# Optimization experiments

Hardware: AMD Instinct MI355X
Metric: run time of the kernel (lower is better)

The kernel has to match this reference:

```python
import jax, jax.numpy as jnp
import numpy as np
import itertools

D_FEAT = 8      # feature dim per point
N_NBR = 16     # kNN neighbors (self.N)
ORDERS = (2, 3)
BIG = 99999999.0


def _to_select(N, order):
    # rows: [0] + each (order-1)-combination of {1..N-1}, first N-1 rows
    rows = [[0] + list(c) for c in itertools.combinations(range(1, N), order - 1)][:N - 1]
    return np.asarray(rows, dtype=np.int32)  # (N-1, order)


def setup_inputs() -> dict:
    key = jax.random.key(0)
    ks = jax.random.split(key, 18)
    B, NP, DM, DO, NM, PNM = 4, 4096, 16, 8, 64, 64
    r = lambda k, s: jax.random.normal(k, s, dtype=jnp.float32)
    return {
        "x": r(ks[0], (B, NP * D_FEAT)),
        "z": r(ks[1], (B, PNM)),
        "Wm2": r(ks[2], (2, DM)) * 0.5, "bm2": r(ks[3], (DM,)) * 0.1,
        "Wm3": r(ks[4], (3, DM)) * 0.5, "bm3": r(ks[5], (DM,)) * 0.1,
        "Wv2": r(ks[6], (2, DM)) * 0.5, "bv2": r(ks[7], (DM,)) * 0.1,
        "Wv3": r(ks[8], (3, DM)) * 0.5, "bv3": r(ks[9], (DM,)) * 0.1,
        "Wmx": r(ks[10], (2 * DM, DO)) * 0.1, "bmx": r(ks[11], (DO,)) * 0.1,
        "Wvx": r(ks[12], (2 * DM, NM)) * 0.1, "bvx": r(ks[13], (NM,)) * 0.1,
        "Wmz": r(ks[14], (PNM, DO)) * 0.1, "bmz": r(ks[15], (DO,)) * 0.1,
        "Wvz": r(ks[16], (PNM, NM)) * 0.1, "bvz": r(ks[17], (NM,)) * 0.1,
    }


def _forward(x, z, Wm2, bm2, Wm3, bm3, Wv2, bv2, Wv3, bv3,
             Wmx, bmx, Wvx, bvx, Wmz, bmz, Wvz, bvz):
    B = x.shape[0]
    NP = x.shape[1] // D_FEAT
    N = N_NBR
    x3 = x.reshape(B, NP, D_FEAT)

    # pairwise euclidean distances via gram trick (avoids B*NP*NP*D intermediate)
    n2 = jnp.sum(x3 * x3, axis=-1)                                   # (B, NP)
    d2 = n2[:, :, None] + n2[:, None, :] - 2.0 * jnp.einsum('bid,bjd->bij', x3, x3)
    dist = jnp.sqrt(jnp.maximum(d2, 0.0))                            # (B, NP, NP)
    dist = jnp.where(dist == 0.0, BIG, dist)                         # mask exact-zero distances
    diag = jnp.arange(NP)
    dist = dist.at[:, diag, diag].set(BIG)                           # self-distance (exactly 0 in torch)

    # N smallest, sorted ascending
    _, idx = jax.lax.top_k(-dist, N)                                 # idx: (B, NP, N)

    def order_feats(Wf, bf, order):
        ts = jnp.asarray(_to_select(N, order))                       # (N-1, order)
        sel = idx[:, :, ts]                                          # (B, NP, N-1, o)
        g = jax.vmap(lambda xb, sb: xb[sb])(x3, sel)                 # (B, NP, N-1, o, D)
        # Linear(order -> d_Mfeat) applied per feature-dim o-tuple, relu, mean over feature dims
        y = jax.nn.relu(jnp.einsum('bnrod,ok->bnrdk', g, Wf) + bf)   # (B, NP, N-1, D, K)
        return y.mean(axis=3).reshape(B, NP * (N - 1), -1)           # (B, NP*(N-1), K)

    moments = jnp.concatenate([order_feats(Wm2, bm2, 2), order_feats(Wm3, bm3, 3)], axis=-1)
    v_moments = jnp.concatenate([order_feats(Wv2, bv2, 2), order_feats(Wv3, bv3, 3)], axis=-1)

    d_out = Wmx.shape[1]
    x_new = jax.nn.relu(moments @ Wmx + bmx + (z @ Wmz + bmz)[:, None, :])
    x_new = x_new.reshape(B, NP, N - 1, d_out).mean(axis=2).reshape(B, NP * d_out)

    z_new = jax.nn.relu(v_moments @ Wvx + bvx + (z @ Wvz + bvz)[:, None, :]).mean(axis=1)
    return x_new, z_new


def reference(x, z, Wm2, bm2, Wm3, bm3, Wv2, bv2, Wv3, bv3,
              Wmx, bmx, Wvx, bvx, Wmz, bmz, Wvz, bvz):
    return _forward(x, z, Wm2, bm2, Wm3, bm3, Wv2, bv2, Wv3, bv3,
                    Wmx, bmx, Wvx, bvx, Wmz, bmz, Wvz, bvz)
```

## Files before the change

### kernel.cpp

```cpp
#include <hip/hip_runtime.h>
#include <hip/hip_bf16.h>

#define NPP 4096
#define BB 4
#define NQ 4
#define CAP 128

typedef float f32x2 __attribute__((ext_vector_type(2)));
typedef unsigned long long u64;

__device__ __forceinline__ f32x2 pk_fma(f32x2 a, f32x2 b, f32x2 c) {
    f32x2 d;
    asm("v_pk_fma_f32 %0, %1, %2, %3" : "=v"(d) : "v"(a), "v"(b), "v"(c));
    return d;
}

template <typename T>
__device__ __forceinline__ T bitonic_sort64(T v, int lane) {
    #pragma unroll
    for (int k = 2; k <= 64; k <<= 1) {
        #pragma unroll
        for (int j = k >> 1; j > 0; j >>= 1) {
            T p = __shfl_xor(v, j);
            bool up  = ((lane & k) == 0);
            bool low = ((lane & j) == 0);
            T mn = (v < p) ? v : p;
            T mx = (v < p) ? p : v;
            v = (up == low) ? mn : mx;
        }
    }
    return v;
}

__device__ __forceinline__ float dot8_pk(const f32x2* qp, f32x2 p0, f32x2 p1,
                                         f32x2 p2, f32x2 p3) {
    f32x2 acc = {0.f, 0.f};
    acc = pk_fma(qp[0], p0, acc);
    acc = pk_fma(qp[1], p1, acc);
    acc = pk_fma(qp[2], p2, acc);
    acc = pk_fma(qp[3], p3, acc);
    return acc.x + acc.y;
}


__global__ __launch_bounds__(256) void n2_kernel(
    const float* __restrict__ x, const float* __restrict__ z,
    const float* __restrict__ Wmz, const float* __restrict__ bmz,
    const float* __restrict__ Wvz, const float* __restrict__ bvz,
    float* __restrict__ n2tab, float* __restrict__ zzm, float* __restrict__ zzv,
    float* __restrict__ zout)
{
    int i = blockIdx.x * 256 + threadIdx.x;
    const float4* p = (const float4*)(x + (long)i * 8);
    float4 a = p[0], c = p[1];
    float s = 0.f;
    s = fmaf(a.x, a.x, s); s = fmaf(a.y, a.y, s);
    s = fmaf(a.z, a.z, s); s = fmaf(a.w, a.w, s);
    s = fmaf(c.x, c.x, s); s = fmaf(c.y, c.y, s);
    s = fmaf(c.z, c.z, s); s = fmaf(c.w, c.w, s);
    n2tab[i] = s;

    if (blockIdx.x == 0) {
        zout[threadIdx.x] = 0.f;
        int b = threadIdx.x >> 6, l = threadIdx.x & 63;
        float sv = 0.f;
        for (int q = 0; q < 64; ++q) sv = fmaf(z[b * 64 + q], Wvz[q * 64 + l], sv);
        zzv[b * 64 + l] = sv + bvz[l];
        if (threadIdx.x < 32) {
            int bm = threadIdx.x >> 3, lm = threadIdx.x & 7;
            float sm = 0.f;
            for (int q = 0; q < 64; ++q) sm = fmaf(z[bm * 64 + q], Wmz[q * 8 + lm], sm);
            zzm[bm * 8 + lm] = sm + bmz[lm];
        }
    }
}


__global__ __launch_bounds__(256) void fused_kernel(
    const float* __restrict__ x, const float* __restrict__ n2tab,
    const float* __restrict__ Wm2, const float* __restrict__ bm2,
    const float* __restrict__ Wm3, const float* __restrict__ bm3,
    const float* __restrict__ Wv2, const float* __restrict__ bv2,
    const float* __restrict__ Wv3, const float* __restrict__ bv3,
    const float* __restrict__ Wmx, const float* __restrict__ bmx,
    const float* __restrict__ Wvx, const float* __restrict__ bvx,
    const float* __restrict__ zzm, const float* __restrict__ zzv,
    float* __restrict__ xout, float* __restrict__ zout)
{
    __shared__ __align__(16) char ubuf[4][4352];
    __shared__ float xg_s[4][NQ][16][8];
    __shared__ int   idx_s[4][NQ][16];
    __shared__ float wmxT_s[8][40];
    __shared__ float bzm_s[8];
    __shared__ float zpart[4][64];
    __shared__ unsigned cnt_s[4][NQ];

    int lane = threadIdx.x & 63;
    int wid  = threadIdx.x >> 6;
    int gw   = blockIdx.x * 4 + wid;
    int q0   = gw * NQ;
    int b    = q0 >> 12;
    int qloc = q0 & 4095;
    const float* xb = x + (long)b * NPP * 8;
    const float* nb = n2tab + b * NPP;

    if (threadIdx.x < 256) wmxT_s[threadIdx.x & 7][threadIdx.x >> 3] = Wmx[threadIdx.x];
    if (threadIdx.x < 8)   bzm_s[threadIdx.x] = bmx[threadIdx.x] + zzm[b * 8 + threadIdx.x];
    if (lane < NQ) cnt_s[wid][lane] = 0;
    __syncthreads();

    f32x2 qp[NQ][4];
    float n2i[NQ];
    int selfT[NQ], selfL[NQ];
    #pragma unroll
    for (int q = 0; q < NQ; ++q) {
        const f32x2* qsrc = (const f32x2*)(xb + (long)(qloc + q) * 8);
        #pragma unroll
        for (int e = 0; e < 4; ++e) qp[q][e] = qsrc[e];
        n2i[q]   = nb[qloc + q];
        selfT[q] = (qloc + q) >> 6;
        selfL[q] = (qloc + q) & 63;
    }

    unsigned minb[NQ];
    #pragma unroll
    for (int q = 0; q < NQ; ++q) minb[q] = 0xFFFFFFFFu;

    #pragma unroll 4
    for (int tt = 0; tt < 32; ++tt) {
        int t = tt * 2;
        int j = t * 64 + lane;
        const f32x2* pj = (const f32x2*)(xb + (long)j * 8);
        f32x2 p0 = pj[0], p1 = pj[1], p2 = pj[2], p3 = pj[3];
        float n2j = nb[j];
        #pragma unroll
        for (int q = 0; q < NQ; ++q) {
            float dot = dot8_pk(qp[q], p0, p1, p2, p3);
            float d2  = fmaf(-2.0f, dot, n2i[q] + n2j);
            unsigned kb = __float_as_uint(d2);
            if (t == selfT[q]) kb = (lane == selfL[q]) ? 0xFFFFFFFFu : kb;
            minb[q] = (kb < minb[q]) ? kb : minb[q];
        }
    }

    unsigned T[NQ];
    #pragma unroll
    for (int q = 0; q < NQ; ++q) {
        unsigned s = bitonic_sort64(minb[q], lane);
        T[q] = (unsigned)__shfl((int)s, 15);
    }

    u64* cand = (u64*)ubuf[wid];
    #pragma unroll 2
    for (int t = 0; t < 64; ++t) {
        int j = t * 64 + lane;
        const f32x2* pj = (const f32x2*)(xb + (long)j * 8);
        f32x2 p0 = pj[0], p1 = pj[1], p2 = pj[2], p3 = pj[3];
        float n2j = nb[j];
        #pragma unroll
        for (int q = 0; q < NQ; ++q) {
            float dot = dot8_pk(qp[q], p0, p1, p2, p3);
            float d2  = fmaf(-2.0f, dot, n2i[q] + n2j);
            unsigned kb = __float_as_uint(d2);
            if (t == selfT[q]) kb = (lane == selfL[q]) ? 0xFFFFFFFFu : kb;
            if (kb <= T[q]) {
                unsigned old = atomicAdd(&cnt_s[wid][q], 1u);
                if (old < CAP) cand[q * CAP + old] = ((u64)kb << 32) | (unsigned)j;
            }
        }
    }

    #pragma unroll 1
    for (int q = 0; q < NQ; ++q) {
        unsigned nc = cnt_s[wid][q];
        int n = nc > CAP ? CAP : (int)nc;
        u64 v = (lane < n) ? cand[q * CAP + lane] : ~0ull;
        u64 R = bitonic_sort64(v, lane);
        if (n > 64) {
            u64 w2 = (64 + lane < n) ? cand[q * CAP + 64 + lane] : ~0ull;
            w2 = bitonic_sort64(w2, lane);
            u64 vt = __shfl(w2, lane - 16);
            u64 comb = (lane < 16) ? R : ((lane < 32) ? vt : ~0ull);
            R = bitonic_sort64(comb, lane);
        }
        if (lane < 16) idx_s[wid][q][lane] = (int)(R & 0xFFFFFFFFull);
    }

    #pragma unroll
    for (int p = 0; p < NQ; ++p) {
        if (lane < 16) {
            int id = idx_s[wid][p][lane];
            const float4* ps = (const float4*)(xb + (long)id * 8);
            float4 A = ps[0], C = ps[1];
            *((float4*)&xg_s[wid][p][lane][0]) = A;
            *((float4*)&xg_s[wid][p][lane][4]) = C;
        }
    }

    int k = lane & 15;
    float w20 = Wm2[k], w21 = Wm2[16 + k], bb2 = bm2[k];
    float w30 = Wm3[k], w31 = Wm3[16 + k], w32 = Wm3[32 + k], bb3 = bm3[k];
    float u20 = Wv2[k], u21 = Wv2[16 + k], cc2 = bv2[k];
    float u30 = Wv3[k], u31 = Wv3[16 + k], u32 = Wv3[32 + k], cc3 = bv3[k];

    int g  = lane >> 5;
    int nm = lane & 31;
    f32x2 wa2[16], wb2[16];
    #pragma unroll
    for (int cc = 0; cc < 16; ++cc) {
        wa2[cc].x = Wvx[(2 * cc) * 64 + nm];
        wa2[cc].y = Wvx[(2 * cc + 1) * 64 + nm];
        wb2[cc].x = Wvx[(2 * cc) * 64 + nm + 32];
        wb2[cc].y = Wvx[(2 * cc + 1) * 64 + nm + 32];
    }
    float bz3a = bvx[nm]      + zzv[b * 64 + nm];
    float bz3b = bvx[nm + 32] + zzv[b * 64 + nm + 32];

    float* mo = (float*)ubuf[wid];
    float Aacc = 0.f, Bacc = 0.f;

    #pragma unroll 1
    for (int p = 0; p < NQ; ++p) {
        float4 g0l = *(const float4*)&xg_s[wid][p][0][0];
        float4 g0h = *(const float4*)&xg_s[wid][p][0][4];
        float g0[8] = {g0l.x, g0l.y, g0l.z, g0l.w, g0h.x, g0h.y, g0h.z, g0h.w};

        #pragma unroll
        for (int pp = 0; pp < 4; ++pp) {
            int rg = lane >> 4;
            int r  = pp * 4 + rg;
            int rc = (r < 14) ? r : 14;
            int i2  = rc + 1;
            int i3a = (rc < 14) ? 1 : 2;
            int i3b = (rc < 14) ? rc + 2 : 3;
            float4 a1 = *(const float4*)&xg_s[wid][p][i2][0];
            float4 b1 = *(const float4*)&xg_s[wid][p][i2][4];
            float4 aa = *(const float4*)&xg_s[wid][p][i3a][0];
            float4 ba = *(const float4*)&xg_s[wid][p][i3a][4];
            float4 ab = *(const float4*)&xg_s[wid][p][i3b][0];
            float4 bb = *(const float4*)&xg_s[wid][p][i3b][4];
            float G1[8]  = {a1.x, a1.y, a1.z, a1.w, b1.x, b1.y, b1.z, b1.w};
            float G3a[8] = {aa.x, aa.y, aa.z, aa.w, ba.x, ba.y, ba.z, ba.w};
            float G3b[8] = {ab.x, ab.y, ab.z, ab.w, bb.x, bb.y, bb.z, bb.w};
            float s2 = 0.f, s3 = 0.f, t2 = 0.f, t3 = 0.f;
            #pragma unroll
            for (int d = 0; d < 8; ++d) {
                float gz = g0[d], g1 = G1[d], ga = G3a[d], gb = G3b[d];
                float y2 = fmaf(gz, w20, fmaf(g1, w21, bb2));
                s2 += fmaxf(y2, 0.f);
                float y3 = fmaf(gz, w30, fmaf(ga, w31, fmaf(gb, w32, bb3)));
                s3 += fmaxf(y3, 0.f);
                float z2 = fmaf(gz, u20, fmaf(g1, u21, cc2));
                t2 += fmaxf(z2, 0.f);
                float z3 = fmaf(gz, u30, fmaf(ga, u31, fmaf(gb, u32, cc3)));
                t3 += fmaxf(z3, 0.f);
            }
            if (r < 15) {
                mo[r * 72 + k]      = s2 * 0.125f;
                mo[r * 72 + 16 + k] = s3 * 0.125f;
                mo[r * 72 + 32 + k] = t2 * 0.125f;
                mo[r * 72 + 48 + k] = t3 * 0.125f;
            }
        }

        float xa = 0.f;
        #pragma unroll
        for (int half = 0; half < 2; ++half) {
            int r   = (lane >> 3) + half * 8;
            int doo = lane & 7;
            if (r < 15) {
                const f32x2* vp = (const f32x2*)&mo[r * 72];
                const f32x2* wp = (const f32x2*)&wmxT_s[doo][0];
                f32x2 acc = {0.f, 0.f};
                #pragma unroll
                for (int cc = 0; cc < 16; ++cc) acc = pk_fma(vp[cc], wp[cc], acc);
                float s = bzm_s[doo] + acc.x + acc.y;
                xa += fmaxf(s, 0.f);
            }
        }
        xa += __shfl_xor(xa, 8);
        xa += __shfl_xor(xa, 16);
        xa += __shfl_xor(xa, 32);
        if (lane < 8) xout[(long)(q0 + p) * 8 + lane] = xa * (1.0f / 15.0f);

        #pragma unroll 1
        for (int rr = 0; rr < 8; ++rr) {
            int r = g * 8 + rr;
            if (r < 15) {
                const f32x2* vp = (const f32x2*)&mo[r * 72 + 32];
                f32x2 accA = {0.f, 0.f}, accB = {0.f, 0.f};
                #pragma unroll
                for (int cc = 0; cc < 16; ++cc) {
                    f32x2 v = vp[cc];
                    accA = pk_fma(v, wa2[cc], accA);
                    accB = pk_fma(v, wb2[cc], accB);
                }
                float sa = bz3a + accA.x + accA.y;
                float sb = bz3b + accB.x + accB.y;
                Aacc += fmaxf(sa, 0.f);
                Bacc += fmaxf(sb, 0.f);
            }
        }
    }

    Aacc += __shfl_xor(Aacc, 32);
    Bacc += __shfl_xor(Bacc, 32);
    float za = ((g == 0) ? Aacc : Bacc) * (1.0f / 61440.0f);
    zpart[wid][lane] = za;
    __syncthreads();
    if (wid == 0) {
        float ssum = zpart[0][lane] + zpart[1][lane] + zpart[2][lane] + zpart[3][lane];
        atomicAdd(&zout[b * 64 + lane], ssum);
    }
}


extern "C" void kernel_launch(void* const* d_in, const int* in_sizes, int n_in,
                              void* d_out, int out_size, void* d_ws, size_t ws_size,
                              hipStream_t stream) {
    const float* x   = (const float*)d_in[0];
    const float* z   = (const float*)d_in[1];
    const float* Wm2 = (const float*)d_in[2];
    const float* bm2 = (const float*)d_in[3];
    const float* Wm3 = (const float*)d_in[4];
    const float* bm3 = (const float*)d_in[5];
    const float* Wv2 = (const float*)d_in[6];
    const float* bv2 = (const float*)d_in[7];
    const float* Wv3 = (const float*)d_in[8];
    const float* bv3 = (const float*)d_in[9];
    const float* Wmx = (const float*)d_in[10];
    const float* bmx = (const float*)d_in[11];
    const float* Wvx = (const float*)d_in[12];
    const float* bvx = (const float*)d_in[13];
    const float* Wmz = (const float*)d_in[14];
    const float* bmz = (const float*)d_in[15];
    const float* Wvz = (const float*)d_in[16];
    const float* bvz = (const float*)d_in[17];

    float* out  = (float*)d_out;
    float* zzm  = (float*)d_ws;
    float* zzv  = zzm + 32;
    float* n2t  = zzv + 256;
    float* xout = out;
    float* zout = out + BB * NPP * 8;

    n2_kernel<<<dim3(BB * NPP / 256), dim3(256), 0, stream>>>(
        x, z, Wmz, bmz, Wvz, bvz, n2t, zzm, zzv, zout);
    fused_kernel<<<dim3(BB * NPP / (4 * NQ)), dim3(256), 0, stream>>>(
        x, n2t, Wm2, bm2, Wm3, bm3, Wv2, bv2, Wv3, bv3,
        Wmx, bmx, Wvx, bvx, zzm, zzv, xout, zout);
}
```

Before: 217.6 us.

## Split each query group's kNN scan across two waves with shared candidate buffers

Each block now holds two waves that share four queries. Each wave scans half of the points and derives its own pruning threshold. Candidates from both halves are merged in shared memory, and each wave then sorts and post-processes two of the queries. This doubles the number of waves so latency hides better and per-wave serial work shrinks. The cost is more candidates per query (capacity raised, with multi-chunk merging), extra block barriers and more global atomics on zout. Point loads switch to float4 and the moments buffer stride is narrowed.

```diff
diff --git a/kernel.cpp b/kernel.cpp
--- a/kernel.cpp
+++ b/kernel.cpp
@@ -4,7 +4,8 @@
 #define NPP 4096
 #define BB 4
 #define NQ 4
-#define CAP 128
+#define CAP 160
+#define MOSTRIDE 66
 
 typedef float f32x2 __attribute__((ext_vector_type(2)));
 typedef unsigned long long u64;
@@ -32,8 +33,9 @@
     return v;
 }
 
-__device__ __forceinline__ float dot8_pk(const f32x2* qp, f32x2 p0, f32x2 p1,
-                                         f32x2 p2, f32x2 p3) {
+__device__ __forceinline__ float dot8_pk(const f32x2* qp, float4 A0, float4 A1) {
+    f32x2 p0 = {A0.x, A0.y}, p1 = {A0.z, A0.w};
+    f32x2 p2 = {A1.x, A1.y}, p3 = {A1.z, A1.w};
     f32x2 acc = {0.f, 0.f};
     acc = pk_fma(qp[0], p0, acc);
     acc = pk_fma(qp[1], p1, acc);
@@ -76,7 +78,7 @@
 }
 
 
-__global__ __launch_bounds__(256) void fused_kernel(
+__global__ __launch_bounds__(128) void fused_kernel(
     const float* __restrict__ x, const float* __restrict__ n2tab,
     const float* __restrict__ Wm2, const float* __restrict__ bm2,
     const float* __restrict__ Wm3, const float* __restrict__ bm3,
@@ -87,27 +89,24 @@
     const float* __restrict__ zzm, const float* __restrict__ zzv,
     float* __restrict__ xout, float* __restrict__ zout)
 {
-    __shared__ __align__(16) char ubuf[4][4352];
-    __shared__ float xg_s[4][NQ][16][8];
-    __shared__ int   idx_s[4][NQ][16];
-    __shared__ float wmxT_s[8][40];
+    __shared__ __align__(16) char ubuf[7936];
+    __shared__ float xg_s[2][2][16][8];
+    __shared__ float wmxT_s[8][36];
     __shared__ float bzm_s[8];
-    __shared__ float zpart[4][64];
-    __shared__ unsigned cnt_s[4][NQ];
+    __shared__ unsigned cnt_s[NQ];
 
     int lane = threadIdx.x & 63;
-    int wid  = threadIdx.x >> 6;
-    int gw   = blockIdx.x * 4 + wid;
-    int q0   = gw * NQ;
+    int wid2 = threadIdx.x >> 6;
+    int q0   = blockIdx.x * NQ;
     int b    = q0 >> 12;
     int qloc = q0 & 4095;
     const float* xb = x + (long)b * NPP * 8;
     const float* nb = n2tab + b * NPP;
 
-    if (threadIdx.x < 256) wmxT_s[threadIdx.x & 7][threadIdx.x >> 3] = Wmx[threadIdx.x];
-    if (threadIdx.x < 8)   bzm_s[threadIdx.x] = bmx[threadIdx.x] + zzm[b * 8 + threadIdx.x];
-    if (lane < NQ) cnt_s[wid][lane] = 0;
-    __syncthreads();
+    for (int i = threadIdx.x; i < 256; i += 128)
+        wmxT_s[i & 7][i >> 3] = Wmx[i];
+    if (threadIdx.x < 8) bzm_s[threadIdx.x] = bmx[threadIdx.x] + zzm[b * 8 + threadIdx.x];
+    if (threadIdx.x < NQ) cnt_s[threadIdx.x] = 0;
 
     f32x2 qp[NQ][4];
     float n2i[NQ];
@@ -122,20 +121,24 @@
         selfL[q] = (qloc + q) & 63;
     }
 
+    __syncthreads();
+
+    int tbase = wid2 * 32;
+
     unsigned minb[NQ];
     #pragma unroll
     for (int q = 0; q < NQ; ++q) minb[q] = 0xFFFFFFFFu;
 
     #pragma unroll 4
-    for (int tt = 0; tt < 32; ++tt) {
-        int t = tt * 2;
+    for (int i = 0; i < 16; ++i) {
+        int t = tbase + (i << 1);
         int j = t * 64 + lane;
-        const f32x2* pj = (const f32x2*)(xb + (long)j * 8);
-        f32x2 p0 = pj[0], p1 = pj[1], p2 = pj[2], p3 = pj[3];
+        const float4* pj = (const float4*)(xb + (long)j * 8);
+        float4 A0 = pj[0], A1 = pj[1];
         float n2j = nb[j];
         #pragma unroll
         for (int q = 0; q < NQ; ++q) {
-            float dot = dot8_pk(qp[q], p0, p1, p2, p3);
+            float dot = dot8_pk(qp[q], A0, A1);
             float d2  = fmaf(-2.0f, dot, n2i[q] + n2j);
             unsigned kb = __float_as_uint(d2);
             if (t == selfT[q]) kb = (lane == selfL[q]) ? 0xFFFFFFFFu : kb;
@@ -150,52 +153,56 @@
         T[q] = (unsigned)__shfl((int)s, 15);
     }
 
-    u64* cand = (u64*)ubuf[wid];
-    #pragma unroll 2
-    for (int t = 0; t < 64; ++t) {
+    u64* cand = (u64*)ubuf;
+    #pragma unroll 4
+    for (int i = 0; i < 32; ++i) {
+        int t = tbase + i;
         int j = t * 64 + lane;
-        const f32x2* pj = (const f32x2*)(xb + (long)j * 8);
-        f32x2 p0 = pj[0], p1 = pj[1], p2 = pj[2], p3 = pj[3];
+        const float4* pj = (const float4*)(xb + (long)j * 8);
+        float4 A0 = pj[0], A1 = pj[1];
         float n2j = nb[j];
         #pragma unroll
         for (int q = 0; q < NQ; ++q) {
-            float dot = dot8_pk(qp[q], p0, p1, p2, p3);
+            float dot = dot8_pk(qp[q], A0, A1);
             float d2  = fmaf(-2.0f, dot, n2i[q] + n2j);
             unsigned kb = __float_as_uint(d2);
             if (t == selfT[q]) kb = (lane == selfL[q]) ? 0xFFFFFFFFu : kb;
             if (kb <= T[q]) {
-                unsigned old = atomicAdd(&cnt_s[wid][q], 1u);
+                unsigned old = atomicAdd(&cnt_s[q], 1u);
                 if (old < CAP) cand[q * CAP + old] = ((u64)kb << 32) | (unsigned)j;
             }
         }
     }
 
+    __syncthreads();
+
     #pragma unroll 1
-    for (int q = 0; q < NQ; ++q) {
-        unsigned nc = cnt_s[wid][q];
+    for (int sub = 0; sub < 2; ++sub) {
+        int qs = wid2 * 2 + sub;
+        unsigned nc = cnt_s[qs];
         int n = nc > CAP ? CAP : (int)nc;
-        u64 v = (lane < n) ? cand[q * CAP + lane] : ~0ull;
+        u64 v = (lane < n) ? cand[qs * CAP + lane] : ~0ull;
         u64 R = bitonic_sort64(v, lane);
-        if (n > 64) {
-            u64 w2 = (64 + lane < n) ? cand[q * CAP + 64 + lane] : ~0ull;
+        int nch = (n + 63) >> 6;
+        #pragma unroll 1
+        for (int c2 = 1; c2 < nch; ++c2) {
+            int base = c2 << 6;
+            u64 w2 = (base + lane < n) ? cand[qs * CAP + base + lane] : ~0ull;
             w2 = bitonic_sort64(w2, lane);
             u64 vt = __shfl(w2, lane - 16);
             u64 comb = (lane < 16) ? R : ((lane < 32) ? vt : ~0ull);
             R = bitonic_sort64(comb, lane);
         }
-        if (lane < 16) idx_s[wid][q][lane] = (int)(R & 0xFFFFFFFFull);
-    }
-
-    #pragma unroll
-    for (int p = 0; p < NQ; ++p) {
         if (lane < 16) {
-            int id = idx_s[wid][p][lane];
+            int id = (int)(R & 0xFFFFFFFFull);
             const float4* ps = (const float4*)(xb + (long)id * 8);
             float4 A = ps[0], C = ps[1];
-            *((float4*)&xg_s[wid][p][lane][0]) = A;
-            *((float4*)&xg_s[wid][p][lane][4]) = C;
-        }
-    }
+            *((float4*)&xg_s[wid2][sub][lane][0]) = A;
+            *((float4*)&xg_s[wid2][sub][lane][4]) = C;
+        }
+    }
+
+    __syncthreads();
 
     int k = lane & 15;
     float w20 = Wm2[k], w21 = Wm2[16 + k], bb2 = bm2[k];
@@ -216,13 +223,14 @@
     float bz3a = bvx[nm]      + zzv[b * 64 + nm];
     float bz3b = bvx[nm + 32] + zzv[b * 64 + nm + 32];
 
-    float* mo = (float*)ubuf[wid];
+    float* mo = (float*)ubuf + wid2 * (15 * MOSTRIDE);
     float Aacc = 0.f, Bacc = 0.f;
 
     #pragma unroll 1
-    for (int p = 0; p < NQ; ++p) {
-        float4 g0l = *(const float4*)&xg_s[wid][p][0][0];
-        float4 g0h = *(const float4*)&xg_s[wid][p][0][4];
+    for (int sub = 0; sub < 2; ++sub) {
+        int pn = q0 + wid2 * 2 + sub;
+        float4 g0l = *(const float4*)&xg_s[wid2][sub][0][0];
+        float4 g0h = *(const float4*)&xg_s[wid2][sub][0][4];
         float g0[8] = {g0l.x, g0l.y, g0l.z, g0l.w, g0h.x, g0h.y, g0h.z, g0h.w};
 
         #pragma unroll
@@ -233,12 +241,12 @@
             int i2  = rc + 1;
             int i3a = (rc < 14) ? 1 : 2;
             int i3b = (rc < 14) ? rc + 2 : 3;
-            float4 a1 = *(const float4*)&xg_s[wid][p][i2][0];
-            float4 b1 = *(const float4*)&xg_s[wid][p][i2][4];
-            float4 aa = *(const float4*)&xg_s[wid][p][i3a][0];
-            float4 ba = *(const float4*)&xg_s[wid][p][i3a][4];
-            float4 ab = *(const float4*)&xg_s[wid][p][i3b][0];
-            float4 bb = *(const float4*)&xg_s[wid][p][i3b][4];
+            float4 a1 = *(const float4*)&xg_s[wid2][sub][i2][0];
+            float4 b1 = *(const float4*)&xg_s[wid2][sub][i2][4];
+            float4 aa = *(const float4*)&xg_s[wid2][sub][i3a][0];
+            float4 ba = *(const float4*)&xg_s[wid2][sub][i3a][4];
+            float4 ab = *(const float4*)&xg_s[wid2][sub][i3b][0];
+            float4 bb = *(const float4*)&xg_s[wid2][sub][i3b][4];
             float G1[8]  = {a1.x, a1.y, a1.z, a1.w, b1.x, b1.y, b1.z, b1.w};
             float G3a[8] = {aa.x, aa.y, aa.z, aa.w, ba.x, ba.y, ba.z, ba.w};
             float G3b[8] = {ab.x, ab.y, ab.z, ab.w, bb.x, bb.y, bb.z, bb.w};
@@ -256,10 +264,10 @@
                 t3 += fmaxf(z3, 0.f);
             }
             if (r < 15) {
-                mo[r * 72 + k]      = s2 * 0.125f;
-                mo[r * 72 + 16 + k] = s3 * 0.125f;
-                mo[r * 72 + 32 + k] = t2 * 0.125f;
-                mo[r * 72 + 48 + k] = t3 * 0.125f;
+                mo[r * MOSTRIDE + k]      = s2 * 0.125f;
+                mo[r * MOSTRIDE + 16 + k] = s3 * 0.125f;
+                mo[r * MOSTRIDE + 32 + k] = t2 * 0.125f;
+                mo[r * MOSTRIDE + 48 + k] = t3 * 0.125f;
             }
         }
 
@@ -269,7 +277,7 @@
             int r   = (lane >> 3) + half * 8;
             int doo = lane & 7;
             if (r < 15) {
-                const f32x2* vp = (const f32x2*)&mo[r * 72];
+                const f32x2* vp = (const f32x2*)&mo[r * MOSTRIDE];
                 const f32x2* wp = (const f32x2*)&wmxT_s[doo][0];
                 f32x2 acc = {0.f, 0.f};
                 #pragma unroll
@@ -281,13 +289,13 @@
         xa += __shfl_xor(xa, 8);
         xa += __shfl_xor(xa, 16);
         xa += __shfl_xor(xa, 32);
-        if (lane < 8) xout[(long)(q0 + p) * 8 + lane] = xa * (1.0f / 15.0f);
+        if (lane < 8) xout[(long)pn * 8 + lane] = xa * (1.0f / 15.0f);
 
         #pragma unroll 1
         for (int rr = 0; rr < 8; ++rr) {
             int r = g * 8 + rr;
             if (r < 15) {
-                const f32x2* vp = (const f32x2*)&mo[r * 72 + 32];
+                const f32x2* vp = (const f32x2*)&mo[r * MOSTRIDE + 32];
                 f32x2 accA = {0.f, 0.f}, accB = {0.f, 0.f};
                 #pragma unroll
                 for (int cc = 0; cc < 16; ++cc) {
@@ -306,12 +314,7 @@
     Aacc += __shfl_xor(Aacc, 32);
     Bacc += __shfl_xor(Bacc, 32);
     float za = ((g == 0) ? Aacc : Bacc) * (1.0f / 61440.0f);
-    zpart[wid][lane] = za;
-    __syncthreads();
-    if (wid == 0) {
-        float ssum = zpart[0][lane] + zpart[1][lane] + zpart[2][lane] + zpart[3][lane];
-        atomicAdd(&zout[b * 64 + lane], ssum);
-    }
+    atomicAdd(&zout[b * 64 + lane], za);
 }
 
 
@@ -346,7 +349,7 @@
 
     n2_kernel<<<dim3(BB * NPP / 256), dim3(256), 0, stream>>>(
         x, z, Wmz, bmz, Wvz, bvz, n2t, zzm, zzv, zout);
-    fused_kernel<<<dim3(BB * NPP / (4 * NQ)), dim3(256), 0, stream>>>(
+    fused_kernel<<<dim3(BB * NPP / NQ), dim3(128), 0, stream>>>(
         x, n2t, Wm2, bm2, Wm3, bm3, Wv2, bv2, Wv3, bv3,
         Wmx, bmx, Wvx, bvx, zzm, zzv, xout, zout);
 }
```

Result: slower. 293.0 us (+34.6%).
